# Kernel optimization log

Hardware: AMD Instinct MI355X
Metric: run time of the kernel (lower is better)

Reference implementation:

```python
import jax, jax.numpy as jnp
import numpy as np

B = 262144
MA = [128, 128]
MB = [128, 128]


def krone_linear(x_a, x_b, wa, wb, ba, bb):
    # slice inputs to each branch's in_features (torch slices the wider branch)
    ia, ib = wa.shape[1], wb.shape[1]
    x_a = x_a[:, :ia]
    x_b = x_b[:, :ib]
    h_a = x_a @ wa.T + ba
    h_b = x_b @ wb.T + bb
    # zero-pad the narrower output so both branches share a width (static shapes)
    oa, ob = wa.shape[0], wb.shape[0]
    if oa > ob:
        h_b = jnp.pad(h_b, ((0, 0), (0, oa - ob)))
    elif ob > oa:
        h_a = jnp.pad(h_a, ((0, 0), (0, ob - oa)))
    return h_a, h_b


def krone_softmax(x_a, x_b, fa, fb):
    x_a = x_a[:, :fa]
    x_b = x_b[:, :fb]
    # vectorized per-row Kronecker product: kron(a, b)[i*fb + j] = a[i]*b[j]
    y = (x_a[:, :, None] * x_b[:, None, :]).reshape(x_a.shape[0], fa * fb)
    return jax.nn.softmax(y, axis=1)


def setup_inputs() -> dict:
    key = jax.random.key(0)
    ks = jax.random.split(key, 13)
    s = 0.1
    inp = {
        "x": jax.random.normal(ks[0], (2, B, 2), dtype=jnp.float32),
        "w1a": jax.random.normal(ks[1], (MA[0], 2), dtype=jnp.float32) * s,
        "w1b": jax.random.normal(ks[2], (MB[0], 2), dtype=jnp.float32) * s,
        "b1a": jax.random.normal(ks[3], (MA[0],), dtype=jnp.float32) * s,
        "b1b": jax.random.normal(ks[4], (MB[0],), dtype=jnp.float32) * s,
        "w2a": jax.random.normal(ks[5], (MA[1], MA[0]), dtype=jnp.float32) * s,
        "w2b": jax.random.normal(ks[6], (MB[1], MB[0]), dtype=jnp.float32) * s,
        "b2a": jax.random.normal(ks[7], (MA[1],), dtype=jnp.float32) * s,
        "b2b": jax.random.normal(ks[8], (MB[1],), dtype=jnp.float32) * s,
        "w3a": jax.random.normal(ks[9], (1, MA[1]), dtype=jnp.float32) * s,
        "w3b": jax.random.normal(ks[10], (3, MB[1]), dtype=jnp.float32) * s,
        "b3a": jax.random.normal(ks[11], (1,), dtype=jnp.float32) * s,
        "b3b": jax.random.normal(ks[12], (3,), dtype=jnp.float32) * s,
    }
    return inp


def reference(x, w1a, w1b, b1a, b1b, w2a, w2b, b2a, b2b, w3a, w3b, b3a, b3b):
    x_a, x_b = x[0], x[1]
    h_a, h_b = krone_linear(x_a, x_b, w1a, w1b, b1a, b1b)
    h_a, h_b = jax.nn.relu(h_a), jax.nn.relu(h_b)
    h_a, h_b = krone_linear(h_a, h_b, w2a, w2b, b2a, b2b)
    h_a, h_b = jax.nn.relu(h_a), jax.nn.relu(h_b)
    h_a, h_b = krone_linear(h_a, h_b, w3a, w3b, b3a, b3b)
    return krone_softmax(h_a, h_b, 1, 3)
```

## Files before the change

### kernel.cpp

```cpp
#include <hip/hip_runtime.h>
#include <hip/hip_bf16.h>


#define BTOT 262144
#define NBLK (BTOT / 512)

typedef __attribute__((ext_vector_type(4))) float floatx4;
typedef __attribute__((ext_vector_type(8))) short bf16x8;
typedef __attribute__((ext_vector_type(4))) int  intx4;

#define OFF_W2    0
#define OFF_W1FA  32768
#define OFF_W1FB  40960
#define OFF_B2A   49152
#define OFF_B2B   49664
#define OFF_W3A   50176
#define OFF_W3T   50688
#define OFF_SA    52736
#define LDS_TOTAL 54784

static __device__ __forceinline__ int pack2bf(float lo, float hi) {
    int r;
    asm("v_cvt_pk_bf16_f32 %0, %1, %2" : "=v"(r) : "v"(lo), "v"(hi));
    return r;
}

template <int CTRL>
static __device__ __forceinline__ float dppadd(float v) {
    int t = __builtin_amdgcn_update_dpp(0, __builtin_bit_cast(int, v),
                                        CTRL, 0xF, 0xF, true);
    return v + __builtin_bit_cast(float, t);
}

static __device__ __forceinline__ float red4(float a0, float a1, float a2,
                                             float a3, int col) {
    float s0 = dppadd<0xB1>(a0), s1 = dppadd<0xB1>(a1);
    float s2 = dppadd<0xB1>(a2), s3 = dppadd<0xB1>(a3);
    float u0 = (col & 1) ? s1 : s0;
    float u1 = (col & 1) ? s3 : s2;
    float v0 = dppadd<0x4E>(u0), v1 = dppadd<0x4E>(u1);
    float w  = (col & 2) ? v1 : v0;
    w = dppadd<0x124>(w);
    w = dppadd<0x128>(w);
    return w;
}

static __device__ __forceinline__ void pack_w2(
        unsigned char* dst, int tid, const float* __restrict__ w2) {
    const float4* w2p = (const float4*)w2;
    #pragma unroll
    for (int i = 0; i < 8; ++i) {
        int n  = (tid & 15) | (i << 4);
        int k4 = tid >> 4;
        float4 f = w2p[n * 32 + k4];
        int k = k4 * 4;
        int s = k >> 5;
        int j0 = k & 7;
        int l = ((k & 31) >> 3) * 16 + (n & 15);
        int2 pkd;
        pkd.x = pack2bf(f.x, f.y);
        pkd.y = pack2bf(f.z, f.w);
        *(int2*)(dst + (s * 8 + (n >> 4)) * 1024 + l * 16 + j0 * 2) = pkd;
    }
}

static __device__ __forceinline__ void stage_w1f(
        unsigned char* smem, int off, int tid,
        const float* __restrict__ w1, const float* __restrict__ b1) {
    int tp = tid >> 6, l = tid & 63;
    intx4 e = (intx4){0, 0, 0, 0};
    if (l < 16) {
        int n1 = (tp >> 1) * 32 + (l >> 2) * 8 + (tp & 1) * 4 + (l & 3);
        float w0 = w1[2 * n1], w1v = w1[2 * n1 + 1], bb = b1[n1];
        int dhi = pack2bf(w0, w1v);
        float w0r = __builtin_bit_cast(float, dhi << 16);
        float w1r = __builtin_bit_cast(float, dhi & 0xffff0000);
        int dlo = pack2bf(w0 - w0r, w1v - w1r);
        int bh  = pack2bf(bb, 0.f);
        float bbr = __builtin_bit_cast(float, bh << 16);
        int dbias = pack2bf(bb, bb - bbr);
        e = (intx4){dhi, dlo, dhi, dbias};
    }
    ((intx4*)(smem + off))[tid] = e;
}

#define GEMM_CHUNK(acc, XF, W1Fp, W2p, B2p)                                    \
    {                                                                          \
        _Pragma("unroll")                                                      \
        for (int t = 0; t < 8; ++t) {                                          \
            float b2n = (B2p)[t * 16 + col];                                   \
            floatx4 bi = (floatx4){b2n, b2n, b2n, b2n};                        \
            _Pragma("unroll")                                                  \
            for (int mt = 0; mt < 2; ++mt) acc[t][mt] = bi;                    \
        }                                                                      \
        const floatx4 zf = (floatx4){0.f, 0.f, 0.f, 0.f};                      \
        _Pragma("unroll")                                                      \
        for (int s = 0; s < 4; ++s) {                                          \
            bf16x8 a0 = (W1Fp)[(2 * s) * 64 + lane];                           \
            bf16x8 a1 = (W1Fp)[(2 * s + 1) * 64 + lane];                       \
            intx4 af[2];                                                       \
            _Pragma("unroll")                                                  \
            for (int mt = 0; mt < 2; ++mt) {                                   \
                floatx4 td0 = __builtin_amdgcn_mfma_f32_16x16x32_bf16(         \
                    a0, __builtin_bit_cast(bf16x8, (XF)[mt]), zf, 0, 0, 0);    \
                floatx4 td1 = __builtin_amdgcn_mfma_f32_16x16x32_bf16(         \
                    a1, __builtin_bit_cast(bf16x8, (XF)[mt]), zf, 0, 0, 0);    \
                af[mt][0] = pack2bf(fmaxf(td0[0], 0.f), fmaxf(td0[1], 0.f));   \
                af[mt][1] = pack2bf(fmaxf(td0[2], 0.f), fmaxf(td0[3], 0.f));   \
                af[mt][2] = pack2bf(fmaxf(td1[0], 0.f), fmaxf(td1[1], 0.f));   \
                af[mt][3] = pack2bf(fmaxf(td1[2], 0.f), fmaxf(td1[3], 0.f));   \
            }                                                                  \
            _Pragma("unroll")                                                  \
            for (int t = 0; t < 8; ++t) {                                      \
                bf16x8 bfr = (W2p)[(s * 8 + t) * 64 + lane];                   \
                _Pragma("unroll")                                              \
                for (int mt = 0; mt < 2; ++mt)                                 \
                    acc[t][mt] = __builtin_amdgcn_mfma_f32_16x16x32_bf16(      \
                        __builtin_bit_cast(bf16x8, af[mt]), bfr,               \
                        acc[t][mt], 0, 0, 0);                                  \
            }                                                                  \
        }                                                                      \
    }

static __device__ __forceinline__ intx4 make_xfrag(float2 xx) {
    int d0 = pack2bf(xx.x, xx.y);
    float r0 = __builtin_bit_cast(float, d0 << 16);
    float r1 = __builtin_bit_cast(float, d0 & 0xffff0000);
    int d2 = pack2bf(xx.x - r0, xx.y - r1);
    return (intx4){d0, d0, d2, 0x3f803f80};
}

__global__ __launch_bounds__(512, 2)
void krone_fused(const float* __restrict__ x,
                 const float* __restrict__ w1a, const float* __restrict__ w1b,
                 const float* __restrict__ b1a, const float* __restrict__ b1b,
                 const float* __restrict__ w2a, const float* __restrict__ w2b,
                 const float* __restrict__ b2a, const float* __restrict__ b2b,
                 const float* __restrict__ w3a, const float* __restrict__ w3b,
                 const float* __restrict__ b3a, const float* __restrict__ b3b,
                 float* __restrict__ out) {
    __shared__ __align__(16) unsigned char smem[LDS_TOTAL];

    const int tid  = threadIdx.x;
    const int lane = tid & 63;
    const int wave = tid >> 6;
    const int quad = lane >> 4;
    const int col  = lane & 15;
    const int wbase = blockIdx.x * 512 + wave * 64;

    const bf16x8* W2   = (const bf16x8*)(smem + OFF_W2);
    const bf16x8* W1FA = (const bf16x8*)(smem + OFF_W1FA);
    const bf16x8* W1FB = (const bf16x8*)(smem + OFF_W1FB);
    const float*  B2A  = (const float*)(smem + OFF_B2A);
    const float*  B2B  = (const float*)(smem + OFF_B2B);
    const float*  W3A  = (const float*)(smem + OFF_W3A);
    const floatx4* W3T = (const floatx4*)(smem + OFF_W3T);
    float*        SA   = (float*)(smem + OFF_SA);
    const float2* xA = (const float2*)x;
    const float2* xB = xA + BTOT;

    const float b3a_ = b3a[0];
    const float b30 = b3b[0], b31 = b3b[1], b32 = b3b[2];

    float2 xv[4];
    #pragma unroll
    for (int c = 0; c < 2; ++c)
        #pragma unroll
        for (int mt = 0; mt < 2; ++mt)
            xv[c * 2 + mt] = xA[wbase + c * 32 + mt * 16 + col];

    pack_w2(smem + OFF_W2, tid, w2a);
    stage_w1f(smem, OFF_W1FA, tid, w1a, b1a);
    stage_w1f(smem, OFF_W1FB, tid, w1b, b1b);
    if (tid < 128) {
        ((float*)(smem + OFF_B2A))[tid] = b2a[tid];
        ((float*)(smem + OFF_B2B))[tid] = b2b[tid];
        ((float*)(smem + OFF_W3A))[tid] = w3a[tid];
    }
    if (tid < 384) {
        int j = tid >> 7, n = tid & 127;
        ((float*)(smem + OFF_W3T))[n * 4 + j] = w3b[tid];
    }
    __syncthreads();

    #pragma unroll
    for (int c = 0; c < 2; ++c) {
        intx4 xf[2];
        #pragma unroll
        for (int mt = 0; mt < 2; ++mt) xf[mt] = make_xfrag(xv[c * 2 + mt]);
        floatx4 acc[8][2];
        GEMM_CHUNK(acc, xf, W1FA, W2, B2A);

        float pa[2][4] = {};
        #pragma unroll
        for (int t = 0; t < 8; ++t) {
            float w3n = W3A[t * 16 + col];
            #pragma unroll
            for (int mt = 0; mt < 2; ++mt)
                #pragma unroll
                for (int r = 0; r < 4; ++r)
                    pa[mt][r] = fmaf(w3n, fmaxf(acc[t][mt][r], 0.f), pa[mt][r]);
        }
        #pragma unroll
        for (int mt = 0; mt < 2; ++mt) {
            float w = red4(pa[mt][0], pa[mt][1], pa[mt][2], pa[mt][3], col);
            if (col < 4) {
                int sl = mt * 16 + quad * 4 + col;
                SA[wave * 64 + c * 32 + sl] = (w + b3a_) * 1.44269504089f;
            }
        }
    }

    #pragma unroll
    for (int c = 0; c < 2; ++c)
        #pragma unroll
        for (int mt = 0; mt < 2; ++mt)
            xv[c * 2 + mt] = xB[wbase + c * 32 + mt * 16 + col];

    __syncthreads();
    pack_w2(smem + OFF_W2, tid, w2b);
    __syncthreads();

    #pragma unroll
    for (int c = 0; c < 2; ++c) {
        intx4 xf[2];
        #pragma unroll
        for (int mt = 0; mt < 2; ++mt) xf[mt] = make_xfrag(xv[c * 2 + mt]);
        floatx4 acc[8][2];
        GEMM_CHUNK(acc, xf, W1FB, W2, B2B);

        #pragma unroll
        for (int mt = 0; mt < 2; ++mt) {
            float p0[4] = {}, p1[4] = {}, p2[4] = {};
            #pragma unroll
            for (int t = 0; t < 8; ++t) {
                floatx4 w3v = W3T[t * 16 + col];
                #pragma unroll
                for (int r = 0; r < 4; ++r) {
                    float h = fmaxf(acc[t][mt][r], 0.f);
                    p0[r] = fmaf(w3v.x, h, p0[r]);
                    p1[r] = fmaf(w3v.y, h, p1[r]);
                    p2[r] = fmaf(w3v.z, h, p2[r]);
                }
            }
            float t0 = red4(p0[0], p0[1], p0[2], p0[3], col) + b30;
            float t1 = red4(p1[0], p1[1], p1[2], p1[3], col) + b31;
            float t2 = red4(p2[0], p2[1], p2[2], p2[3], col) + b32;
            if (col < 4) {
                int sl = mt * 16 + quad * 4 + col;
                float sa = SA[wave * 64 + c * 32 + sl];
                float y0 = sa * t0, y1 = sa * t1, y2 = sa * t2;
                float m = fmaxf(y0, fmaxf(y1, y2));
                float e0 = exp2f(y0 - m), e1 = exp2f(y1 - m), e2 = exp2f(y2 - m);
                float rs = __builtin_amdgcn_rcpf(e0 + e1 + e2);
                long o = (long)(wbase + c * 32 + sl) * 3;
                out[o]     = e0 * rs;
                out[o + 1] = e1 * rs;
                out[o + 2] = e2 * rs;
            }
        }
    }
}

extern "C" void kernel_launch(void* const* d_in, const int* in_sizes, int n_in,
                              void* d_out, int out_size, void* d_ws, size_t ws_size,
                              hipStream_t stream) {
    const float* x   = (const float*)d_in[0];
    const float* w1a = (const float*)d_in[1];
    const float* w1b = (const float*)d_in[2];
    const float* b1a = (const float*)d_in[3];
    const float* b1b = (const float*)d_in[4];
    const float* w2a = (const float*)d_in[5];
    const float* w2b = (const float*)d_in[6];
    const float* b2a = (const float*)d_in[7];
    const float* b2b = (const float*)d_in[8];
    const float* w3a = (const float*)d_in[9];
    const float* w3b = (const float*)d_in[10];
    const float* b3a = (const float*)d_in[11];
    const float* b3b = (const float*)d_in[12];
    float* out = (float*)d_out;

    krone_fused<<<NBLK, 512, 0, stream>>>(x, w1a, w1b, b1a, b1b, w2a, w2b,
                                          b2a, b2b, w3a, w3b, b3a, b3b, out);
}
```

Baseline: 105.8 us.

## Split each 64-row tile's layer-2 output columns across a wave pair

Each 64-row tile is now handled by a pair of waves, and each wave computes half of the 128 layer-2 output columns. This halves the per-wave accumulator registers so more waves fit per CU. The block grows to 1024 threads, and the launch bounds are raised to match. Partial layer-3 dot products go through LDS and are combined after extra __syncthreads, which adds LDS traffic, a barrier, and repeats of the layer-1 MFMAs in both waves of a pair.

Result: slower. 287.8 us (+172.1%).

```diff
diff --git a/kernel.cpp b/kernel.cpp
--- a/kernel.cpp
+++ b/kernel.cpp
@@ -16,8 +16,9 @@
 #define OFF_B2B   49664
 #define OFF_W3A   50176
 #define OFF_W3T   50688
-#define OFF_SA    52736
-#define LDS_TOTAL 54784
+#define OFF_PA    52736
+#define OFF_TB    56832
+#define LDS_TOTAL 69120
 
 static __device__ __forceinline__ int pack2bf(float lo, float hi) {
     int r;
@@ -49,9 +50,9 @@
         unsigned char* dst, int tid, const float* __restrict__ w2) {
     const float4* w2p = (const float4*)w2;
     #pragma unroll
-    for (int i = 0; i < 8; ++i) {
-        int n  = (tid & 15) | (i << 4);
-        int k4 = tid >> 4;
+    for (int i = 0; i < 4; ++i) {
+        int n  = (tid & 15) | ((((tid >> 9) << 2) + i) << 4);
+        int k4 = (tid >> 4) & 31;
         float4 f = w2p[n * 32 + k4];
         int k = k4 * 4;
         int s = k >> 5;
@@ -64,10 +65,10 @@
     }
 }
 
-static __device__ __forceinline__ void stage_w1f(
-        unsigned char* smem, int off, int tid,
+static __device__ __forceinline__ void stage_w1f_entry(
+        unsigned char* smem, int off, int t2,
         const float* __restrict__ w1, const float* __restrict__ b1) {
-    int tp = tid >> 6, l = tid & 63;
+    int tp = t2 >> 6, l = t2 & 63;
     intx4 e = (intx4){0, 0, 0, 0};
     if (l < 16) {
         int n1 = (tp >> 1) * 32 + (l >> 2) * 8 + (tp & 1) * 4 + (l & 3);
@@ -81,43 +82,41 @@
         int dbias = pack2bf(bb, bb - bbr);
         e = (intx4){dhi, dlo, dhi, dbias};
     }
-    ((intx4*)(smem + off))[tid] = e;
-}
-
-#define GEMM_CHUNK(acc, XF, W1Fp, W2p, B2p)                                    \
+    ((intx4*)(smem + off))[t2] = e;
+}
+
+#define GEMM_CHUNK_H(acc, XF, W1Fp, W2p, B2p, TB0)                             \
     {                                                                          \
         _Pragma("unroll")                                                      \
-        for (int t = 0; t < 8; ++t) {                                          \
-            float b2n = (B2p)[t * 16 + col];                                   \
+        for (int tt = 0; tt < 4; ++tt) {                                       \
+            float b2n = (B2p)[((TB0) + tt) * 16 + col];                        \
             floatx4 bi = (floatx4){b2n, b2n, b2n, b2n};                        \
             _Pragma("unroll")                                                  \
-            for (int mt = 0; mt < 2; ++mt) acc[t][mt] = bi;                    \
+            for (int mt = 0; mt < 2; ++mt) acc[tt][mt] = bi;                   \
         }                                                                      \
         const floatx4 zf = (floatx4){0.f, 0.f, 0.f, 0.f};                      \
         _Pragma("unroll")                                                      \
         for (int s = 0; s < 4; ++s) {                                          \
             bf16x8 a0 = (W1Fp)[(2 * s) * 64 + lane];                           \
             bf16x8 a1 = (W1Fp)[(2 * s + 1) * 64 + lane];                       \
-            intx4 af[2];                                                       \
             _Pragma("unroll")                                                  \
             for (int mt = 0; mt < 2; ++mt) {                                   \
                 floatx4 td0 = __builtin_amdgcn_mfma_f32_16x16x32_bf16(         \
                     a0, __builtin_bit_cast(bf16x8, (XF)[mt]), zf, 0, 0, 0);    \
                 floatx4 td1 = __builtin_amdgcn_mfma_f32_16x16x32_bf16(         \
                     a1, __builtin_bit_cast(bf16x8, (XF)[mt]), zf, 0, 0, 0);    \
-                af[mt][0] = pack2bf(fmaxf(td0[0], 0.f), fmaxf(td0[1], 0.f));   \
-                af[mt][1] = pack2bf(fmaxf(td0[2], 0.f), fmaxf(td0[3], 0.f));   \
-                af[mt][2] = pack2bf(fmaxf(td1[0], 0.f), fmaxf(td1[1], 0.f));   \
-                af[mt][3] = pack2bf(fmaxf(td1[2], 0.f), fmaxf(td1[3], 0.f));   \
-            }                                                                  \
-            _Pragma("unroll")                                                  \
-            for (int t = 0; t < 8; ++t) {                                      \
-                bf16x8 bfr = (W2p)[(s * 8 + t) * 64 + lane];                   \
+                intx4 af;                                                      \
+                af[0] = pack2bf(fmaxf(td0[0], 0.f), fmaxf(td0[1], 0.f));       \
+                af[1] = pack2bf(fmaxf(td0[2], 0.f), fmaxf(td0[3], 0.f));       \
+                af[2] = pack2bf(fmaxf(td1[0], 0.f), fmaxf(td1[1], 0.f));       \
+                af[3] = pack2bf(fmaxf(td1[2], 0.f), fmaxf(td1[3], 0.f));       \
                 _Pragma("unroll")                                              \
-                for (int mt = 0; mt < 2; ++mt)                                 \
-                    acc[t][mt] = __builtin_amdgcn_mfma_f32_16x16x32_bf16(      \
-                        __builtin_bit_cast(bf16x8, af[mt]), bfr,               \
-                        acc[t][mt], 0, 0, 0);                                  \
+                for (int tt = 0; tt < 4; ++tt) {                               \
+                    bf16x8 bfr = (W2p)[(s * 8 + (TB0) + tt) * 64 + lane];      \
+                    acc[tt][mt] = __builtin_amdgcn_mfma_f32_16x16x32_bf16(     \
+                        __builtin_bit_cast(bf16x8, af), bfr,                   \
+                        acc[tt][mt], 0, 0, 0);                                 \
+                }                                                              \
             }                                                                  \
         }                                                                      \
     }
@@ -130,7 +129,7 @@
     return (intx4){d0, d0, d2, 0x3f803f80};
 }
 
-__global__ __launch_bounds__(512, 2)
+__global__ __launch_bounds__(1024, 8)
 void krone_fused(const float* __restrict__ x,
                  const float* __restrict__ w1a, const float* __restrict__ w1b,
                  const float* __restrict__ b1a, const float* __restrict__ b1b,
@@ -144,9 +143,12 @@
     const int tid  = threadIdx.x;
     const int lane = tid & 63;
     const int wave = tid >> 6;
+    const int pair = wave >> 1;
+    const int hh   = wave & 1;
     const int quad = lane >> 4;
     const int col  = lane & 15;
-    const int wbase = blockIdx.x * 512 + wave * 64;
+    const int pbase = blockIdx.x * 512 + pair * 64;
+    const int tb0   = hh * 4;
 
     const bf16x8* W2   = (const bf16x8*)(smem + OFF_W2);
     const bf16x8* W1FA = (const bf16x8*)(smem + OFF_W1FA);
@@ -155,7 +157,8 @@
     const float*  B2B  = (const float*)(smem + OFF_B2B);
     const float*  W3A  = (const float*)(smem + OFF_W3A);
     const floatx4* W3T = (const floatx4*)(smem + OFF_W3T);
-    float*        SA   = (float*)(smem + OFF_SA);
+    float*        PAf  = (float*)(smem + OFF_PA);
+    float*        TBf  = (float*)(smem + OFF_TB);
     const float2* xA = (const float2*)x;
     const float2* xB = xA + BTOT;
 
@@ -167,11 +170,11 @@
     for (int c = 0; c < 2; ++c)
         #pragma unroll
         for (int mt = 0; mt < 2; ++mt)
-            xv[c * 2 + mt] = xA[wbase + c * 32 + mt * 16 + col];
+            xv[c * 2 + mt] = xA[pbase + c * 32 + mt * 16 + col];
 
     pack_w2(smem + OFF_W2, tid, w2a);
-    stage_w1f(smem, OFF_W1FA, tid, w1a, b1a);
-    stage_w1f(smem, OFF_W1FB, tid, w1b, b1b);
+    if (tid < 512) stage_w1f_entry(smem, OFF_W1FA, tid, w1a, b1a);
+    else           stage_w1f_entry(smem, OFF_W1FB, tid - 512, w1b, b1b);
     if (tid < 128) {
         ((float*)(smem + OFF_B2A))[tid] = b2a[tid];
         ((float*)(smem + OFF_B2B))[tid] = b2b[tid];
@@ -188,26 +191,24 @@
         intx4 xf[2];
         #pragma unroll
         for (int mt = 0; mt < 2; ++mt) xf[mt] = make_xfrag(xv[c * 2 + mt]);
-        floatx4 acc[8][2];
-        GEMM_CHUNK(acc, xf, W1FA, W2, B2A);
+        floatx4 acc[4][2];
+        GEMM_CHUNK_H(acc, xf, W1FA, W2, B2A, tb0);
 
         float pa[2][4] = {};
         #pragma unroll
-        for (int t = 0; t < 8; ++t) {
-            float w3n = W3A[t * 16 + col];
+        for (int tt = 0; tt < 4; ++tt) {
+            float w3n = W3A[(tb0 + tt) * 16 + col];
             #pragma unroll
             for (int mt = 0; mt < 2; ++mt)
                 #pragma unroll
                 for (int r = 0; r < 4; ++r)
-                    pa[mt][r] = fmaf(w3n, fmaxf(acc[t][mt][r], 0.f), pa[mt][r]);
+                    pa[mt][r] = fmaf(w3n, fmaxf(acc[tt][mt][r], 0.f), pa[mt][r]);
         }
         #pragma unroll
         for (int mt = 0; mt < 2; ++mt) {
             float w = red4(pa[mt][0], pa[mt][1], pa[mt][2], pa[mt][3], col);
-            if (col < 4) {
-                int sl = mt * 16 + quad * 4 + col;
-                SA[wave * 64 + c * 32 + sl] = (w + b3a_) * 1.44269504089f;
-            }
+            if (col < 4)
+                PAf[(((pair * 2 + c) * 2 + hh) * 2 + mt) * 16 + quad * 4 + col] = w;
         }
     }
 
@@ -215,10 +216,19 @@
     for (int c = 0; c < 2; ++c)
         #pragma unroll
         for (int mt = 0; mt < 2; ++mt)
-            xv[c * 2 + mt] = xB[wbase + c * 32 + mt * 16 + col];
+            xv[c * 2 + mt] = xB[pbase + c * 32 + mt * 16 + col];
 
     __syncthreads();
+
     pack_w2(smem + OFF_W2, tid, w2b);
+
+    float sa[2];
+    #pragma unroll
+    for (int mt = 0; mt < 2; ++mt) {
+        int i0 = (((pair * 2 + hh) * 2 + 0) * 2 + mt) * 16 + quad * 4 + (col & 3);
+        int i1 = (((pair * 2 + hh) * 2 + 1) * 2 + mt) * 16 + quad * 4 + (col & 3);
+        sa[mt] = (PAf[i0] + PAf[i1] + b3a_) * 1.44269504089f;
+    }
     __syncthreads();
 
     #pragma unroll
@@ -226,38 +236,54 @@
         intx4 xf[2];
         #pragma unroll
         for (int mt = 0; mt < 2; ++mt) xf[mt] = make_xfrag(xv[c * 2 + mt]);
-        floatx4 acc[8][2];
-        GEMM_CHUNK(acc, xf, W1FB, W2, B2B);
+        floatx4 acc[4][2];
+        GEMM_CHUNK_H(acc, xf, W1FB, W2, B2B, tb0);
 
         #pragma unroll
         for (int mt = 0; mt < 2; ++mt) {
             float p0[4] = {}, p1[4] = {}, p2[4] = {};
             #pragma unroll
-            for (int t = 0; t < 8; ++t) {
-                floatx4 w3v = W3T[t * 16 + col];
+            for (int tt = 0; tt < 4; ++tt) {
+                floatx4 w3v = W3T[(tb0 + tt) * 16 + col];
                 #pragma unroll
                 for (int r = 0; r < 4; ++r) {
-                    float h = fmaxf(acc[t][mt][r], 0.f);
-                    p0[r] = fmaf(w3v.x, h, p0[r]);
-                    p1[r] = fmaf(w3v.y, h, p1[r]);
-                    p2[r] = fmaf(w3v.z, h, p2[r]);
+                    float hv = fmaxf(acc[tt][mt][r], 0.f);
+                    p0[r] = fmaf(w3v.x, hv, p0[r]);
+                    p1[r] = fmaf(w3v.y, hv, p1[r]);
+                    p2[r] = fmaf(w3v.z, hv, p2[r]);
                 }
             }
-            float t0 = red4(p0[0], p0[1], p0[2], p0[3], col) + b30;
-            float t1 = red4(p1[0], p1[1], p1[2], p1[3], col) + b31;
-            float t2 = red4(p2[0], p2[1], p2[2], p2[3], col) + b32;
+            float t0 = red4(p0[0], p0[1], p0[2], p0[3], col);
+            float t1 = red4(p1[0], p1[1], p1[2], p1[3], col);
+            float t2 = red4(p2[0], p2[1], p2[2], p2[3], col);
             if (col < 4) {
-                int sl = mt * 16 + quad * 4 + col;
-                float sa = SA[wave * 64 + c * 32 + sl];
-                float y0 = sa * t0, y1 = sa * t1, y2 = sa * t2;
-                float m = fmaxf(y0, fmaxf(y1, y2));
-                float e0 = exp2f(y0 - m), e1 = exp2f(y1 - m), e2 = exp2f(y2 - m);
-                float rs = __builtin_amdgcn_rcpf(e0 + e1 + e2);
-                long o = (long)(wbase + c * 32 + sl) * 3;
-                out[o]     = e0 * rs;
-                out[o + 1] = e1 * rs;
-                out[o + 2] = e2 * rs;
+                int base = ((((pair * 2 + c) * 2 + hh) * 2 + mt) * 3);
+                TBf[(base + 0) * 16 + quad * 4 + col] = t0;
+                TBf[(base + 1) * 16 + quad * 4 + col] = t1;
+                TBf[(base + 2) * 16 + quad * 4 + col] = t2;
             }
+        }
+    }
+    __syncthreads();
+
+    #pragma unroll
+    for (int mt = 0; mt < 2; ++mt) {
+        int idx = quad * 4 + (col & 3);
+        int b0 = (((pair * 2 + hh) * 2 + 0) * 2 + mt) * 3;
+        int b1 = (((pair * 2 + hh) * 2 + 1) * 2 + mt) * 3;
+        float t0 = TBf[(b0 + 0) * 16 + idx] + TBf[(b1 + 0) * 16 + idx] + b30;
+        float t1 = TBf[(b0 + 1) * 16 + idx] + TBf[(b1 + 1) * 16 + idx] + b31;
+        float t2 = TBf[(b0 + 2) * 16 + idx] + TBf[(b1 + 2) * 16 + idx] + b32;
+        float y0 = sa[mt] * t0, y1 = sa[mt] * t1, y2 = sa[mt] * t2;
+        float m = fmaxf(y0, fmaxf(y1, y2));
+        float e0 = exp2f(y0 - m), e1 = exp2f(y1 - m), e2 = exp2f(y2 - m);
+        float rs = __builtin_amdgcn_rcpf(e0 + e1 + e2);
+        if (col < 4) {
+            int sl = mt * 16 + quad * 4 + col;
+            long o = (long)(pbase + hh * 32 + sl) * 3;
+            out[o]     = e0 * rs;
+            out[o + 1] = e1 * rs;
+            out[o + 2] = e2 * rs;
         }
     }
 }
@@ -280,6 +306,6 @@
     const float* b3b = (const float*)d_in[12];
     float* out = (float*)d_out;
 
-    krone_fused<<<NBLK, 512, 0, stream>>>(x, w1a, w1b, b1a, b1b, w2a, w2b,
-                                          b2a, b2b, w3a, w3b, b3a, b3b, out);
-}
+    krone_fused<<<NBLK, 1024, 0, stream>>>(x, w1a, w1b, b1a, b1b, w2a, w2b,
+                                           b2a, b2b, w3a, w3b, b3a, b3b, out);
+}
```
